# Kernel tuning notes

Hardware: AMD Instinct MI355X
Metric: run time of the kernel (lower is better)

## Reference

```python
import jax, jax.numpy as jnp
import numpy as np

B, L, D, CH, H = 16384, 50, 20, 16, 6


def setup_inputs() -> dict:
    key = jax.random.key(0)
    ks = jax.random.split(key, 18)
    s = 0.1
    return {
        "x": jax.random.normal(ks[0], (B, L, D), jnp.float32),
        "we_w": jax.random.normal(ks[1], (CH, D), jnp.float32) * s,
        "we_b": jax.random.normal(ks[2], (CH,), jnp.float32) * s,
        "attn_w": jax.random.normal(ks[3], (CH, CH), jnp.float32) * s,
        "attn_b": jax.random.normal(ks[4], (CH,), jnp.float32) * s,
        "conv1_w": jax.random.normal(ks[5], (CH, CH, 1), jnp.float32) * s,
        "conv1_b": jax.random.normal(ks[6], (CH,), jnp.float32) * s,
        "conv2_w": jax.random.normal(ks[7], (CH, CH, 3), jnp.float32) * s,
        "conv2_b": jax.random.normal(ks[8], (CH,), jnp.float32) * s,
        "conv3_w": jax.random.normal(ks[9], (CH, CH, 5), jnp.float32) * s,
        "conv3_b": jax.random.normal(ks[10], (CH,), jnp.float32) * s,
        "gru_wih": jax.random.normal(ks[11], (3 * H, CH), jnp.float32) * s,
        "gru_whh": jax.random.normal(ks[12], (3 * H, H), jnp.float32) * s,
        "gru_bih": jax.random.normal(ks[13], (3 * H,), jnp.float32) * s,
        "gru_bhh": jax.random.normal(ks[14], (3 * H,), jnp.float32) * s,
        "fc3_w": jax.random.normal(ks[15], (2, 3 * CH + H), jnp.float32) * s,
        "fc3_b": jax.random.normal(ks[16], (2,), jnp.float32) * s,
        "batchsize": B,
    }


def _conv1d(x, w, b, pad):
    # x: [B, C, L], w: [O, I, K] -> [B, O, L]
    y = jax.lax.conv_general_dilated(x, w, (1,), [(pad, pad)],
                                     dimension_numbers=("NCH", "OIH", "NCH"))
    return y + b[None, :, None]


def _gru(xg, wih, whh, bih, bhh):
    # xg: [B, L, CH] -> outputs [B, L, H] (PyTorch GRU equations, h0=0)
    gi = jnp.einsum("blc,gc->blg", xg, wih) + bih  # [B, L, 3H]
    gi_t = jnp.swapaxes(gi, 0, 1)                  # [L, B, 3H]
    h0 = jnp.zeros((xg.shape[0], H), xg.dtype)

    def step(h, gi_step):
        gh = h @ whh.T + bhh
        i_r, i_z, i_n = jnp.split(gi_step, 3, axis=-1)
        h_r, h_z, h_n = jnp.split(gh, 3, axis=-1)
        r = jax.nn.sigmoid(i_r + h_r)
        z = jax.nn.sigmoid(i_z + h_z)
        n = jnp.tanh(i_n + r * h_n)
        h_new = (1.0 - z) * n + z * h
        return h_new, h_new

    _, outs = jax.lax.scan(step, h0, gi_t)
    return jnp.swapaxes(outs, 0, 1)  # [B, L, H]


def reference(x, we_w, we_b, attn_w, attn_b, conv1_w, conv1_b, conv2_w, conv2_b,
              conv3_w, conv3_b, gru_wih, gru_whh, gru_bih, gru_bhh, fc3_w, fc3_b,
              batchsize):
    b = batchsize
    xe = x @ we_w.T + we_b                 # [B, L, CH]
    xr = xe.reshape(b, CH, L)              # RESHAPE (not transpose), as in torch

    lrelu = lambda v: jnp.where(v > 0, v, 0.1 * v)
    x1 = lrelu(_conv1d(xr, conv1_w, conv1_b, 0))
    x2 = lrelu(_conv1d(xr, conv2_w, conv2_b, 1))
    x3 = lrelu(_conv1d(xr, conv3_w, conv3_b, 2))

    xg = xr.reshape(b, L, CH)              # == xe
    x4 = _gru(xg, gru_wih, gru_whh, gru_bih, gru_bhh)  # [B, L, H]

    # dotproduct1: note x4.reshape([B,H,L]) is a reshape, NOT a transpose
    scores = jnp.matmul(x4, x4.reshape(b, H, L)) / H   # [B, L, L]
    alphas = jax.nn.softmax(scores, axis=1)            # softmax over dim=1 as in torch
    y = jnp.matmul(alphas, x4).reshape(b, H, L)        # [B, H, L]
    x_gru = jnp.sum(y, axis=2)                         # [B, H]

    # vectorized per-timestep attention loop: x[:, :, i] over i -> swapaxes
    xt = jnp.swapaxes(xr, 1, 2)                        # [B, L, CH]
    attn = jnp.tanh(xt @ attn_w.T + attn_b)            # [B, L, CH]
    attn1 = jnp.concatenate([attn, attn, attn], axis=2).reshape(b, 3 * CH, L)

    x_cat = jnp.concatenate([x1, x2, x3], axis=1)      # [B, 3CH, L]
    x_cnn = jnp.sum(x_cat * attn1, axis=2)             # [B, 3CH]

    feat = jnp.concatenate([x_cnn, x_gru], axis=1)     # [B, 3CH+H]
    return feat @ fc3_w.T + fc3_b                      # [B, 2]
```

## Files before the change

kernel.cpp:

```cpp
#include <hip/hip_runtime.h>

#define BATCH 16384
#define LSEQ  50
#define DIN   20
#define CHN   16
#define HID   6

typedef float vf2 __attribute__((ext_vector_type(2)));

__device__ __forceinline__ float frcp(float x){ return __builtin_amdgcn_rcpf(x); }
__device__ __forceinline__ float fsig(float x){ return frcp(1.0f + __expf(-x)); }
__device__ __forceinline__ float ftanh(float x){ float t = __expf(2.0f*x); return (t - 1.0f) * frcp(t + 1.0f); }
__device__ __forceinline__ float lrelu(float v){ return v > 0.0f ? v : 0.1f*v; }
__device__ __forceinline__ vf2 fma2(vf2 a, vf2 b, vf2 c){
#if __has_builtin(__builtin_elementwise_fma)
  return __builtin_elementwise_fma(a, b, c);
#else
  vf2 r; r.x = fmaf(a.x, b.x, c.x); r.y = fmaf(a.y, b.y, c.y); return r;
#endif
}

constexpr int SLAB = 2544;

__global__ __launch_bounds__(256, 4) void fused_kernel(
    const float* __restrict__ x,
    const float* __restrict__ we_w, const float* __restrict__ we_b,
    const float* __restrict__ attn_w, const float* __restrict__ attn_b,
    const float* __restrict__ c1w, const float* __restrict__ c1b,
    const float* __restrict__ c2w, const float* __restrict__ c2b,
    const float* __restrict__ c3w, const float* __restrict__ c3b,
    const float* __restrict__ wih, const float* __restrict__ whh,
    const float* __restrict__ bih, const float* __restrict__ bhh,
    const float* __restrict__ fc3w, const float* __restrict__ fc3b,
    float* __restrict__ out)
{
  __shared__ __align__(16) float smem[4 * SLAB];
  const int tid  = threadIdx.x;
  const int wave = tid >> 6;
  const int lane = tid & 63;
  const int b    = blockIdx.x * 4 + wave;

  float* S    = smem + wave * SLAB;
  float* sXEp = S;
  float* sY   = S;
  float* R1   = S + 840;
  float* sFE  = S + 1640;
  float* sX4  = S + 1840;
  float* sX4P = S + 2144;

  const float* xb = x + (size_t)b * (LSEQ * DIN);

  if (lane < CHN) {
    sXEp[lane * 52]     = 0.0f;
    sXEp[lane * 52 + 1] = 0.0f;
  } else if (lane == 16) {
    sXEp[832] = 0.0f;
    sXEp[833] = 0.0f;
  }

  if (lane < LSEQ) {
    vf2 xv2[10];
    const float4* xr = (const float4*)(xb + lane * DIN);
    #pragma unroll
    for (int q = 0; q < 5; ++q) {
      float4 v = xr[q];
      vf2 p0; p0.x = v.x; p0.y = v.y;
      vf2 p1; p1.x = v.z; p1.y = v.w;
      xv2[2*q] = p0; xv2[2*q+1] = p1;
    }
    float xe[CHN];
    #pragma unroll
    for (int c = 0; c < CHN; ++c) {
      const vf2* wr = (const vf2*)(we_w + c * DIN);
      vf2 a2; a2.x = we_b[c]; a2.y = 0.0f;
      #pragma unroll
      for (int dp = 0; dp < 10; ++dp) a2 = fma2(xv2[dp], wr[dp], a2);
      xe[c] = a2.x + a2.y;
    }
    const int kk0 = lane * CHN;
    const int i0  = kk0 / 50;
    const int m0  = kk0 - i0 * 50;
    float* basep = sXEp + i0 * 52 + 2 + m0;
    #pragma unroll
    for (int c = 0; c < CHN; ++c) {
      const int off = c + ((m0 + c >= 50) ? 2 : 0);
      basep[off] = xe[c];
    }
    vf2 xe2[8];
    #pragma unroll
    for (int p = 0; p < 8; ++p) { xe2[p].x = xe[2*p]; xe2[p].y = xe[2*p+1]; }
    float gi[18];
    #pragma unroll
    for (int g = 0; g < 18; ++g) {
      const vf2* wr = (const vf2*)(wih + g * CHN);
      vf2 a2; a2.x = bih[g]; a2.y = 0.0f;
      #pragma unroll
      for (int p = 0; p < 8; ++p) a2 = fma2(xe2[p], wr[p], a2);
      gi[g] = a2.x + a2.y;
    }
    float4* gd = (float4*)(R1 + lane * 20);
    gd[0] = make_float4(gi[0], gi[1], gi[2], gi[3]);
    gd[1] = make_float4(gi[4], gi[5], gi[6], gi[7]);
    gd[2] = make_float4(gi[8], gi[9], gi[10], gi[11]);
    gd[3] = make_float4(gi[12], gi[13], gi[14], gi[15]);
    *(float2*)(R1 + lane * 20 + 16) = make_float2(gi[16], gi[17]);
  }
  __syncthreads();

  if (wave == 0) {
    const int q = lane >> 4;
    const int g = lane & 15;
    const int gb = 16 + (g & 1);
    float wa[HID], wb[HID];
    #pragma unroll
    for (int k = 0; k < HID; ++k) { wa[k] = whh[g * HID + k]; wb[k] = whh[gb * HID + k]; }
    const float ba = bhh[g];
    const float bb = bhh[gb];

    float* giq  = smem + q * SLAB + 840;
    float* x4q  = smem + q * SLAB + 1840;
    float* x4pq = smem + q * SLAB + 2144;

    const int base = q << 4;
    const int srcZ = base + 6 + g;
    const int srcN = base + ((g < 4) ? (12 + g) : (g - 4));

    float hh[HID];
    #pragma unroll
    for (int k = 0; k < HID; ++k) hh[k] = 0.0f;

    for (int l = 0; l < LSEQ; ++l) {
      const float gia = giq[l * 20 + g];
      const float gib = giq[l * 20 + gb];
      float gha = ba, ghb = bb;
      #pragma unroll
      for (int k = 0; k < HID; ++k) {
        gha = fmaf(wa[k], hh[k], gha);
        ghb = fmaf(wb[k], hh[k], ghb);
      }
      const float siga = fsig(gia + gha);
      const float ghx = (g >= 12) ? gha : ghb;
      const float gix = (g >= 12) ? gia : gib;
      const float ghn = __shfl(ghx, srcN);
      const float gin = __shfl(gix, srcN);
      const float z   = __shfl(siga, srcZ);
      const float n   = ftanh(fmaf(siga, ghn, gin));
      const float hn  = fmaf(z, hh[g < HID ? g : 0] - n, n);
      if (g < HID) {
        x4q[l * HID + g] = hn;
        x4pq[l * 8 + g]  = hn;
      }
      #pragma unroll
      for (int k = 0; k < HID; ++k) hh[k] = __shfl(hn, base + k);
    }
  }
  __syncthreads();

  if (lane < LSEQ) {
    float a[CHN];
    #pragma unroll
    for (int cc = 0; cc < CHN; ++cc) a[cc] = sXEp[cc * 52 + 2 + lane];
    vf2 a2[8];
    #pragma unroll
    for (int p = 0; p < 8; ++p) { a2[p].x = a[2*p]; a2[p].y = a[2*p+1]; }
    float o[CHN];
    #pragma unroll
    for (int c = 0; c < CHN; ++c) {
      const vf2* wr = (const vf2*)(attn_w + c * CHN);
      vf2 s2; s2.x = attn_b[c]; s2.y = 0.0f;
      #pragma unroll
      for (int p = 0; p < 8; ++p) s2 = fma2(a2[p], wr[p], s2);
      o[c] = ftanh(s2.x + s2.y);
    }
    float4* ad = (float4*)(R1 + lane * CHN);
    ad[0] = make_float4(o[0], o[1], o[2], o[3]);
    ad[1] = make_float4(o[4], o[5], o[6], o[7]);
    ad[2] = make_float4(o[8], o[9], o[10], o[11]);
    ad[3] = make_float4(o[12], o[13], o[14], o[15]);
  }
  __syncthreads();

  {
    float* sAT = R1;
    const int o   = lane & 15;
    const int seg = lane >> 4;
    const int s   = seg * 12;
    const int NL  = (seg == 3) ? 14 : 12;
    vf2 Z1[7], Z2[7], Z3[7];
    #pragma unroll
    for (int p = 0; p < 7; ++p) {
      Z1[p] = (vf2)0.0f; Z2[p] = (vf2)0.0f; Z3[p] = (vf2)0.0f;
    }
    for (int i = 0; i < CHN; ++i) {
      const float w1s = c1w[o * CHN + i];
      vf2 W1; W1.x = w1s; W1.y = w1s;
      vf2 W2[3], W3[5];
      #pragma unroll
      for (int t = 0; t < 3; ++t) { float w = c2w[(o * CHN + i) * 3 + t]; W2[t].x = w; W2[t].y = w; }
      #pragma unroll
      for (int t = 0; t < 5; ++t) { float w = c3w[(o * CHN + i) * 5 + t]; W3[t].x = w; W3[t].y = w; }
      const float4* wp = (const float4*)(sXEp + i * 52 + s);
      float4 q0 = wp[0], q1 = wp[1], q2 = wp[2], q3 = wp[3], q4 = wp[4];
      float xv[20] = {q0.x,q0.y,q0.z,q0.w, q1.x,q1.y,q1.z,q1.w,
                      q2.x,q2.y,q2.z,q2.w, q3.x,q3.y,q3.z,q3.w,
                      q4.x,q4.y,q4.z,q4.w};
      vf2 XP[17];
      #pragma unroll
      for (int a = 0; a < 17; ++a) { XP[a].x = xv[a]; XP[a].y = xv[a+1]; }
      #pragma unroll
      for (int p = 0; p < 7; ++p) {
        Z1[p] = fma2(W1, XP[2*p + 2], Z1[p]);
        Z2[p] = fma2(W2[0], XP[2*p + 1], Z2[p]);
        Z2[p] = fma2(W2[1], XP[2*p + 2], Z2[p]);
        Z2[p] = fma2(W2[2], XP[2*p + 3], Z2[p]);
        Z3[p] = fma2(W3[0], XP[2*p    ], Z3[p]);
        Z3[p] = fma2(W3[1], XP[2*p + 1], Z3[p]);
        Z3[p] = fma2(W3[2], XP[2*p + 2], Z3[p]);
        Z3[p] = fma2(W3[3], XP[2*p + 3], Z3[p]);
        Z3[p] = fma2(W3[4], XP[2*p + 4], Z3[p]);
      }
    }
    const float b1v = c1b[o], b2v = c2b[o], b3v = c3b[o];
    float a1 = 0.0f, a2 = 0.0f, a3 = 0.0f;
    #pragma unroll
    for (int u = 0; u < 14; ++u) {
      if (u < NL) {
        int l = s + u;
        float v1 = lrelu(Z1[u >> 1][u & 1] + b1v);
        float v2 = lrelu(Z2[u >> 1][u & 1] + b2v);
        float v3 = lrelu(Z3[u >> 1][u & 1] + b3v);
        int f1 = o * LSEQ + l;
        int f2 = (CHN + o) * LSEQ + l;
        int f3 = (2 * CHN + o) * LSEQ + l;
        a1 += v1 * sAT[(f1 / 48) * CHN + ((f1 % 48) & 15)];
        a2 += v2 * sAT[(f2 / 48) * CHN + ((f2 % 48) & 15)];
        a3 += v3 * sAT[(f3 / 48) * CHN + ((f3 % 48) & 15)];
      }
    }
    a1 += __shfl_xor(a1, 16); a1 += __shfl_xor(a1, 32);
    a2 += __shfl_xor(a2, 16); a2 += __shfl_xor(a2, 32);
    a3 += __shfl_xor(a3, 16); a3 += __shfl_xor(a3, 32);
    if (lane < CHN) { sFE[o] = a1; sFE[CHN + o] = a2; sFE[2 * CHN + o] = a3; }
  }
  __syncthreads();

  float* sC = R1;
  if (lane < LSEQ) {
    float colj[HID];
    #pragma unroll
    for (int h = 0; h < HID; ++h) colj[h] = sX4[h * LSEQ + lane];
    vf2 cj2[3];
    #pragma unroll
    for (int p = 0; p < 3; ++p) { cj2[p].x = colj[2*p]; cj2[p].y = colj[2*p+1]; }
    *(float4*)(sC + lane * 16)     = make_float4(colj[0], colj[1], colj[2], colj[3]);
    *(float2*)(sC + lane * 16 + 4) = make_float2(colj[4], colj[5]);
    float zs = 0.0f;
    for (int i = 0; i < LSEQ; ++i) {
      const float4 r0 = *(const float4*)(sX4P + i * 8);
      const float2 r1 = *(const float2*)(sX4P + i * 8 + 4);
      vf2 p0; p0.x = r0.x; p0.y = r0.y;
      vf2 p1; p1.x = r0.z; p1.y = r0.w;
      vf2 p2; p2.x = r1.x; p2.y = r1.y;
      vf2 s2 = (vf2)0.0f;
      s2 = fma2(p0, cj2[0], s2);
      s2 = fma2(p1, cj2[1], s2);
      s2 = fma2(p2, cj2[2], s2);
      zs += __expf((s2.x + s2.y) * (1.0f / 6.0f));
    }
    const float zi = frcp(zs);
    const float4 q0 = *(const float4*)(sX4P + lane * 8);
    const float2 q1 = *(const float2*)(sX4P + lane * 8 + 4);
    *(float4*)(sC + lane * 16 + 8)  = make_float4(zi*q0.x, zi*q0.y, zi*q0.z, zi*q0.w);
    *(float2*)(sC + lane * 16 + 12) = make_float2(zi*q1.x, zi*q1.y);
  }
  __syncthreads();

  if (lane < LSEQ) {
    vf2 ri2[3];
    {
      const float4 q0 = *(const float4*)(sX4P + lane * 8);
      const float2 q1 = *(const float2*)(sX4P + lane * 8 + 4);
      ri2[0].x = q0.x; ri2[0].y = q0.y;
      ri2[1].x = q0.z; ri2[1].y = q0.w;
      ri2[2].x = q1.x; ri2[2].y = q1.y;
    }
    vf2 ya2[3];
    #pragma unroll
    for (int p = 0; p < 3; ++p) ya2[p] = (vf2)0.0f;
    for (int j = 0; j < LSEQ; ++j) {
      const float4 t0 = *(const float4*)(sC + j * 16);
      const float2 t1 = *(const float2*)(sC + j * 16 + 4);
      vf2 p0; p0.x = t0.x; p0.y = t0.y;
      vf2 p1; p1.x = t0.z; p1.y = t0.w;
      vf2 p2; p2.x = t1.x; p2.y = t1.y;
      vf2 s2 = (vf2)0.0f;
      s2 = fma2(ri2[0], p0, s2);
      s2 = fma2(ri2[1], p1, s2);
      s2 = fma2(ri2[2], p2, s2);
      const float e = __expf((s2.x + s2.y) * (1.0f / 6.0f));
      vf2 e2; e2.x = e; e2.y = e;
      const float4 w0 = *(const float4*)(sC + j * 16 + 8);
      const float2 w1 = *(const float2*)(sC + j * 16 + 12);
      vf2 wv0; wv0.x = w0.x; wv0.y = w0.y;
      vf2 wv1; wv1.x = w0.z; wv1.y = w0.w;
      vf2 wv2; wv2.x = w1.x; wv2.y = w1.y;
      ya2[0] = fma2(e2, wv0, ya2[0]);
      ya2[1] = fma2(e2, wv1, ya2[1]);
      ya2[2] = fma2(e2, wv2, ya2[2]);
    }
    *(float2*)(sY + lane * 6)     = make_float2(ya2[0].x, ya2[0].y);
    *(float2*)(sY + lane * 6 + 2) = make_float2(ya2[1].x, ya2[1].y);
    *(float2*)(sY + lane * 6 + 4) = make_float2(ya2[2].x, ya2[2].y);
  }
  __syncthreads();

  if (lane < HID) {
    float s = 0.0f;
    for (int m = 0; m < LSEQ; ++m) s += sY[lane * LSEQ + m];
    sFE[48 + lane] = s;
  }
  __syncthreads();

  if (lane < 2) {
    float acc = fc3b[lane];
    const float* wr = fc3w + lane * 54;
    #pragma unroll
    for (int k = 0; k < 54; ++k) acc = fmaf(wr[k], sFE[k], acc);
    out[(size_t)b * 2 + lane] = acc;
  }
}

extern "C" void kernel_launch(void* const* d_in, const int* in_sizes, int n_in,
                              void* d_out, int out_size, void* d_ws, size_t ws_size,
                              hipStream_t stream) {
  (void)in_sizes; (void)n_in; (void)d_ws; (void)ws_size; (void)out_size;
  fused_kernel<<<BATCH / 4, 256, 0, stream>>>(
      (const float*)d_in[0],
      (const float*)d_in[1],  (const float*)d_in[2],
      (const float*)d_in[3],  (const float*)d_in[4],
      (const float*)d_in[5],  (const float*)d_in[6],
      (const float*)d_in[7],  (const float*)d_in[8],
      (const float*)d_in[9],  (const float*)d_in[10],
      (const float*)d_in[11], (const float*)d_in[12],
      (const float*)d_in[13], (const float*)d_in[14],
      (const float*)d_in[15], (const float*)d_in[16],
      (float*)d_out);
}
```

Before: 290.8 us.

## Replace block barriers with wave fences, shrink LDS slab, parallelize final reductions

Replaces the later __syncthreads calls with a per-wave LDS wait, since those stages only touch the wave's own slab, leaving block barriers only around the shared GRU stage. It drops the padded duplicate GRU output buffer and packs the gate inputs at stride 18, which shrinks the per-wave slab and lets launch bounds request 5 blocks per CU. It also prefetches the next step's gate inputs in the GRU loop, and replaces the serial final sum and fc3 dot product with shuffle reductions. It relies on lockstep execution within a wave for correctness across the fenced stages.

After: 282.0 us. 1.03x faster.

```diff
diff --git a/kernel.cpp b/kernel.cpp
--- a/kernel.cpp
+++ b/kernel.cpp
@@ -20,9 +20,11 @@
 #endif
 }
 
-constexpr int SLAB = 2544;
-
-__global__ __launch_bounds__(256, 4) void fused_kernel(
+#define WAVE_FENCE() asm volatile("s_waitcnt lgkmcnt(0)" ::: "memory")
+
+constexpr int SLAB = 2040;
+
+__global__ __launch_bounds__(256, 5) void fused_kernel(
     const float* __restrict__ x,
     const float* __restrict__ we_w, const float* __restrict__ we_b,
     const float* __restrict__ attn_w, const float* __restrict__ attn_b,
@@ -45,8 +47,7 @@
   float* sY   = S;
   float* R1   = S + 840;
   float* sFE  = S + 1640;
-  float* sX4  = S + 1840;
-  float* sX4P = S + 2144;
+  float* sX4  = S + 1740;
 
   const float* xb = x + (size_t)b * (LSEQ * DIN);
 
@@ -98,12 +99,9 @@
       for (int p = 0; p < 8; ++p) a2 = fma2(xe2[p], wr[p], a2);
       gi[g] = a2.x + a2.y;
     }
-    float4* gd = (float4*)(R1 + lane * 20);
-    gd[0] = make_float4(gi[0], gi[1], gi[2], gi[3]);
-    gd[1] = make_float4(gi[4], gi[5], gi[6], gi[7]);
-    gd[2] = make_float4(gi[8], gi[9], gi[10], gi[11]);
-    gd[3] = make_float4(gi[12], gi[13], gi[14], gi[15]);
-    *(float2*)(R1 + lane * 20 + 16) = make_float2(gi[16], gi[17]);
+    float2* gd = (float2*)(R1 + lane * 18);
+    #pragma unroll
+    for (int p = 0; p < 9; ++p) gd[p] = make_float2(gi[2*p], gi[2*p+1]);
   }
   __syncthreads();
 
@@ -117,9 +115,8 @@
     const float ba = bhh[g];
     const float bb = bhh[gb];
 
-    float* giq  = smem + q * SLAB + 840;
-    float* x4q  = smem + q * SLAB + 1840;
-    float* x4pq = smem + q * SLAB + 2144;
+    const float* giq = smem + q * SLAB + 840;
+    float* x4q       = smem + q * SLAB + 1740;
 
     const int base = q << 4;
     const int srcZ = base + 6 + g;
@@ -129,27 +126,30 @@
     #pragma unroll
     for (int k = 0; k < HID; ++k) hh[k] = 0.0f;
 
+    const float* gp = giq;
+    float gia = gp[g];
+    float gib = gp[gb];
     for (int l = 0; l < LSEQ; ++l) {
-      const float gia = giq[l * 20 + g];
-      const float gib = giq[l * 20 + gb];
+      const float gia_c = gia;
+      const float gib_c = gib;
+      gp += 18;
+      gia = gp[g];
+      gib = gp[gb];
       float gha = ba, ghb = bb;
       #pragma unroll
       for (int k = 0; k < HID; ++k) {
         gha = fmaf(wa[k], hh[k], gha);
         ghb = fmaf(wb[k], hh[k], ghb);
       }
-      const float siga = fsig(gia + gha);
+      const float siga = fsig(gia_c + gha);
       const float ghx = (g >= 12) ? gha : ghb;
-      const float gix = (g >= 12) ? gia : gib;
+      const float gix = (g >= 12) ? gia_c : gib_c;
       const float ghn = __shfl(ghx, srcN);
       const float gin = __shfl(gix, srcN);
       const float z   = __shfl(siga, srcZ);
       const float n   = ftanh(fmaf(siga, ghn, gin));
       const float hn  = fmaf(z, hh[g < HID ? g : 0] - n, n);
-      if (g < HID) {
-        x4q[l * HID + g] = hn;
-        x4pq[l * 8 + g]  = hn;
-      }
+      if (g < HID) x4q[l * HID + g] = hn;
       #pragma unroll
       for (int k = 0; k < HID; ++k) hh[k] = __shfl(hn, base + k);
     }
@@ -178,7 +178,7 @@
     ad[2] = make_float4(o[8], o[9], o[10], o[11]);
     ad[3] = make_float4(o[12], o[13], o[14], o[15]);
   }
-  __syncthreads();
+  WAVE_FENCE();
 
   {
     float* sAT = R1;
@@ -242,7 +242,7 @@
     a3 += __shfl_xor(a3, 16); a3 += __shfl_xor(a3, 32);
     if (lane < CHN) { sFE[o] = a1; sFE[CHN + o] = a2; sFE[2 * CHN + o] = a3; }
   }
-  __syncthreads();
+  WAVE_FENCE();
 
   float* sC = R1;
   if (lane < LSEQ) {
@@ -256,11 +256,12 @@
     *(float2*)(sC + lane * 16 + 4) = make_float2(colj[4], colj[5]);
     float zs = 0.0f;
     for (int i = 0; i < LSEQ; ++i) {
-      const float4 r0 = *(const float4*)(sX4P + i * 8);
-      const float2 r1 = *(const float2*)(sX4P + i * 8 + 4);
+      const float2 r0 = *(const float2*)(sX4 + i * 6);
+      const float2 r1 = *(const float2*)(sX4 + i * 6 + 2);
+      const float2 r2 = *(const float2*)(sX4 + i * 6 + 4);
       vf2 p0; p0.x = r0.x; p0.y = r0.y;
-      vf2 p1; p1.x = r0.z; p1.y = r0.w;
-      vf2 p2; p2.x = r1.x; p2.y = r1.y;
+      vf2 p1; p1.x = r1.x; p1.y = r1.y;
+      vf2 p2; p2.x = r2.x; p2.y = r2.y;
       vf2 s2 = (vf2)0.0f;
       s2 = fma2(p0, cj2[0], s2);
       s2 = fma2(p1, cj2[1], s2);
@@ -268,21 +269,23 @@
       zs += __expf((s2.x + s2.y) * (1.0f / 6.0f));
     }
     const float zi = frcp(zs);
-    const float4 q0 = *(const float4*)(sX4P + lane * 8);
-    const float2 q1 = *(const float2*)(sX4P + lane * 8 + 4);
-    *(float4*)(sC + lane * 16 + 8)  = make_float4(zi*q0.x, zi*q0.y, zi*q0.z, zi*q0.w);
-    *(float2*)(sC + lane * 16 + 12) = make_float2(zi*q1.x, zi*q1.y);
-  }
-  __syncthreads();
+    const float2 q0 = *(const float2*)(sX4 + lane * 6);
+    const float2 q1 = *(const float2*)(sX4 + lane * 6 + 2);
+    const float2 q2 = *(const float2*)(sX4 + lane * 6 + 4);
+    *(float4*)(sC + lane * 16 + 8)  = make_float4(zi*q0.x, zi*q0.y, zi*q1.x, zi*q1.y);
+    *(float2*)(sC + lane * 16 + 12) = make_float2(zi*q2.x, zi*q2.y);
+  }
+  WAVE_FENCE();
 
   if (lane < LSEQ) {
     vf2 ri2[3];
     {
-      const float4 q0 = *(const float4*)(sX4P + lane * 8);
-      const float2 q1 = *(const float2*)(sX4P + lane * 8 + 4);
+      const float2 q0 = *(const float2*)(sX4 + lane * 6);
+      const float2 q1 = *(const float2*)(sX4 + lane * 6 + 2);
+      const float2 q2 = *(const float2*)(sX4 + lane * 6 + 4);
       ri2[0].x = q0.x; ri2[0].y = q0.y;
-      ri2[1].x = q0.z; ri2[1].y = q0.w;
-      ri2[2].x = q1.x; ri2[2].y = q1.y;
+      ri2[1].x = q1.x; ri2[1].y = q1.y;
+      ri2[2].x = q2.x; ri2[2].y = q2.y;
     }
     vf2 ya2[3];
     #pragma unroll
@@ -312,21 +315,35 @@
     *(float2*)(sY + lane * 6 + 2) = make_float2(ya2[1].x, ya2[1].y);
     *(float2*)(sY + lane * 6 + 4) = make_float2(ya2[2].x, ya2[2].y);
   }
-  __syncthreads();
-
-  if (lane < HID) {
+  WAVE_FENCE();
+
+  if (lane < 48) {
+    const int h = lane >> 3;
+    const int m = lane & 7;
     float s = 0.0f;
-    for (int m = 0; m < LSEQ; ++m) s += sY[lane * LSEQ + m];
-    sFE[48 + lane] = s;
-  }
-  __syncthreads();
-
-  if (lane < 2) {
-    float acc = fc3b[lane];
-    const float* wr = fc3w + lane * 54;
-    #pragma unroll
-    for (int k = 0; k < 54; ++k) acc = fmaf(wr[k], sFE[k], acc);
-    out[(size_t)b * 2 + lane] = acc;
+    #pragma unroll
+    for (int k = 0; k < 7; ++k) {
+      const int idx = m + (k << 3);
+      if (idx < LSEQ) s += sY[h * LSEQ + idx];
+    }
+    s += __shfl_xor(s, 1);
+    s += __shfl_xor(s, 2);
+    s += __shfl_xor(s, 4);
+    if (m == 0) sFE[48 + h] = s;
+  }
+  WAVE_FENCE();
+
+  {
+    const int oo = lane & 1;
+    const int kk = lane >> 1;
+    float s = fc3w[oo * 54 + kk] * sFE[kk];
+    if (kk < 22) s = fmaf(fc3w[oo * 54 + kk + 32], sFE[kk + 32], s);
+    s += __shfl_xor(s, 2);
+    s += __shfl_xor(s, 4);
+    s += __shfl_xor(s, 8);
+    s += __shfl_xor(s, 16);
+    s += __shfl_xor(s, 32);
+    if (lane < 2) out[(size_t)b * 2 + lane] = s + fc3b[lane];
   }
 }
 
```
